# Performance work log

Measured on AMD Instinct MI355X. Metric: run time of the kernel, lower is better.

The kernel has to match this reference:

```python
import jax, jax.numpy as jnp
import numpy as np
import math

SIM_THRESHOLD = 0.05


def setup_inputs() -> dict:
    key = jax.random.key(0)
    ks = jax.random.split(key, 5)
    B, N, D = 32, 65, 512  # N = seq_len + 1
    gain = 1.0 / math.sqrt(2.0)
    lim = gain * math.sqrt(6.0 / (D + D))  # xavier_uniform with gain 1/sqrt(2)
    c = 1.0 / math.sqrt(D)
    return {
        "desc_embeddings": jax.random.normal(ks[0], (B, N - 1, D), jnp.float32),
        "name_value_embeddings": jax.random.normal(ks[1], (B, N, D), jnp.float32),
        "Wq": jax.random.uniform(ks[2], (D, D), jnp.float32, -lim, lim),
        "bq": jnp.zeros((D,), jnp.float32),
        "Wk": jax.random.uniform(ks[3], (D, D), jnp.float32, -lim, lim),
        "bk": jnp.zeros((D,), jnp.float32),
        "cls": jax.random.uniform(ks[4], (D,), jnp.float32, -c, c),
    }


def reference(desc_embeddings, name_value_embeddings, Wq, bq, Wk, bk, cls):
    # desc_embeddings is accepted but unused, exactly as in the torch module.
    nve = name_value_embeddings
    B, N, D = nve.shape
    S = N - 1

    q = nve @ Wq.T + bq  # [B, N, D]
    k = nve @ Wk.T + bk  # [B, N, D]
    attn = jnp.einsum('bid,bjd->bij', q, k) / math.sqrt(D)  # [B, N, N]

    # no_self_loop: multiplicatively zero the diagonal of the [1:,1:] block (pre-softmax)
    mask = jnp.ones((N, N), attn.dtype).at[1:, 1:].set(1.0 - jnp.eye(S, dtype=attn.dtype))
    attn = jax.nn.softmax(attn * mask, axis=-1)

    # row i's subgraph = {i} U {j : attn[b, i, j] > thr, j >= 1}
    members_all = (attn[:, 1:, 1:] > SIM_THRESHOLD) | jnp.eye(S, dtype=bool)  # [B, S, S]

    # Greedy sequential clustering: row i starts a subgraph only if node i is not
    # already used; its members then get marked used. Implemented with lax.scan
    # carrying the per-batch `used` bitmap (replaces the Python set loop).
    def step(used, xs):
        i, members = xs  # members: [B, S] for row i
        active = ~used[:, i]  # [B] -> is node (i+1) unused, i.e. this row is a leader
        sel = members & active[:, None]
        return used | sel, (active, sel)

    used0 = jnp.zeros((B, S), bool)
    _, (leader, member) = jax.lax.scan(
        step, used0, (jnp.arange(S), members_all.swapaxes(0, 1))
    )
    leader = leader.T.astype(nve.dtype)            # [B, S]
    member = member.transpose(1, 0, 2).astype(nve.dtype)  # [B, S, S]

    # Padded representation of the ragged output: for each leader row i,
    # slot 0 = cls token, slots 1..S = member embeddings (index order == sorted order),
    # zeros elsewhere. (out, leader_mask, member_mask) losslessly encode the
    # original list-of-lists of variable-size subgraphs.
    body = nve[:, None, 1:, :] * member[..., None]        # [B, S, S, D]
    cls_part = leader[:, :, None, None] * cls             # [B, S, 1, D]
    out = jnp.concatenate([cls_part, body], axis=2)       # [B, S, S+1, D]
    return out, leader, member
```

## Files before the change

### kernel.cpp

```cpp
#include <hip/hip_runtime.h>
#include <math.h>

constexpr int B = 32;
constexpr int N = 65;
constexpr int D = 512;
constexpr int S = 64;
constexpr int M = B * N;

constexpr size_t OUT0_ELEMS = (size_t)B * S * (S + 1) * D;
constexpr size_t Q_ELEMS    = (size_t)M * D;
constexpr size_t KT_ELEMS   = (size_t)B * D * N;
constexpr size_t STAGE_BASE = OUT0_ELEMS - Q_ELEMS - KT_ELEMS;
constexpr int OUT0_F4 = (int)(OUT0_ELEMS / 4);

constexpr int F_A = 6291456;
constexpr int F_B = 10485760;
constexpr int ROW_F4 = (S + 1) * (D / 4);
constexpr int ROWS_SCATTER = 1383;
constexpr int F_C = ROW_F4 * ROWS_SCATTER;

constexpr int NG_GEMM = 528;
constexpr int NG_FILL = 1536;
constexpr int N2_ATTN = 512;
constexpr int N2_FILL = 768;
constexpr int N3_FILL = 255;
constexpr int N4_DENSE = 2048;
constexpr int N4_TAIL  = 130;

__global__ __launch_bounds__(256) void k1_gemm_fill(
    const float* __restrict__ nve, const float* __restrict__ Wq,
    const float* __restrict__ bq, const float* __restrict__ Wk,
    const float* __restrict__ bk, float* __restrict__ out)
{
    __shared__ float As[32][68];
    __shared__ float Ws[32][68];

    const int gid = blockIdx.x;
    const int tid = threadIdx.x;

    if (gid < NG_GEMM) {
        const int mat = gid >= (NG_GEMM / 2);
        const int t   = mat ? gid - NG_GEMM / 2 : gid;
        const int bm  = (t % 33) * 64;
        const int bn  = (t / 33) * 64;
        const float* W    = mat ? Wk : Wq;
        const float* bias = mat ? bk : bq;

        float* q  = out + STAGE_BASE;
        float* kT = q + Q_ELEMS;

        const int tr = tid / 16;
        const int tc = tid % 16;
        float acc[4][4] = {};

        for (int k0 = 0; k0 < D; k0 += 32) {
            const int r  = tid / 8;
            const int c4 = (tid % 8) * 4;
            #pragma unroll
            for (int p = 0; p < 2; ++p) {
                const int rr = p * 32 + r;
                const int gm = bm + rr;
                float4 v = make_float4(0.f, 0.f, 0.f, 0.f);
                if (gm < M) v = *(const float4*)&nve[(size_t)gm * D + k0 + c4];
                As[c4 + 0][rr] = v.x; As[c4 + 1][rr] = v.y;
                As[c4 + 2][rr] = v.z; As[c4 + 3][rr] = v.w;
                float4 w = *(const float4*)&W[(size_t)(bn + rr) * D + k0 + c4];
                Ws[c4 + 0][rr] = w.x; Ws[c4 + 1][rr] = w.y;
                Ws[c4 + 2][rr] = w.z; Ws[c4 + 3][rr] = w.w;
            }
            __syncthreads();

            #pragma unroll
            for (int kk = 0; kk < 32; ++kk) {
                float a[4], w[4];
                #pragma unroll
                for (int u = 0; u < 4; ++u) a[u] = As[kk][tr * 4 + u];
                #pragma unroll
                for (int u = 0; u < 4; ++u) w[u] = Ws[kk][tc * 4 + u];
                #pragma unroll
                for (int i = 0; i < 4; ++i)
                    #pragma unroll
                    for (int j = 0; j < 4; ++j)
                        acc[i][j] += a[i] * w[j];
            }
            __syncthreads();
        }

        #pragma unroll
        for (int i = 0; i < 4; ++i) {
            const int gm = bm + tr * 4 + i;
            if (gm >= M) continue;
            const int b = gm / N;
            const int n = gm % N;
            if (mat == 0) {
                float4 v;
                v.x = acc[i][0] + bias[bn + tc * 4 + 0];
                v.y = acc[i][1] + bias[bn + tc * 4 + 1];
                v.z = acc[i][2] + bias[bn + tc * 4 + 2];
                v.w = acc[i][3] + bias[bn + tc * 4 + 3];
                *(float4*)&q[(size_t)gm * D + bn + tc * 4] = v;
            } else {
                #pragma unroll
                for (int j = 0; j < 4; ++j) {
                    const int gd = bn + tc * 4 + j;
                    kT[(size_t)b * D * N + (size_t)gd * N + n] = acc[i][j] + bias[gd];
                }
            }
        }
    } else {
        const float4 z = make_float4(0.f, 0.f, 0.f, 0.f);
        float4* o4 = (float4*)out;
        const int nthr = NG_FILL * 256;
        for (int f = (gid - NG_GEMM) * 256 + tid; f < F_A; f += nthr)
            o4[f] = z;
    }
}

__global__ __launch_bounds__(256) void k2_attn(
    const float* __restrict__ out, unsigned long long* __restrict__ mem,
    float* __restrict__ outw)
{
    const int gid = blockIdx.x;
    const int t = threadIdx.x;

    if (gid < N2_ATTN) {
        const float* q  = out + STAGE_BASE;
        const float* kT = q + Q_ELEMS;

        const int b = gid / 16;
        const int rbase = (gid % 16) * 4;

        __shared__ float qrow[4][D];
        __shared__ float sc[4][N];

        #pragma unroll
        for (int w = 0; w < 4; ++w) {
            if (t < 128) {
                const int i = rbase + w + 1;
                *(float4*)&qrow[w][t * 4] =
                    *(const float4*)&q[((size_t)b * N + i) * D + t * 4];
            }
        }
        __syncthreads();

        if (t < N) {
            const float* kp = &kT[(size_t)b * D * N];
            float a0 = 0.f, a1 = 0.f, a2 = 0.f, a3 = 0.f;
            for (int e = 0; e < D; ++e) {
                const float kv = kp[(size_t)e * N + t];
                a0 += qrow[0][e] * kv;
                a1 += qrow[1][e] * kv;
                a2 += qrow[2][e] * kv;
                a3 += qrow[3][e] * kv;
            }
            const float c = 0.044194173824159216f;
            float s0 = a0 * c, s1 = a1 * c, s2 = a2 * c, s3 = a3 * c;
            if (t == rbase + 1) s0 = 0.f;
            if (t == rbase + 2) s1 = 0.f;
            if (t == rbase + 3) s2 = 0.f;
            if (t == rbase + 4) s3 = 0.f;
            sc[0][t] = s0; sc[1][t] = s1; sc[2][t] = s2; sc[3][t] = s3;
        }
        __syncthreads();

        {
            const int w = t >> 6;
            const int lane = t & 63;
            const int i = rbase + w + 1;
            float mx = -INFINITY;
            for (int j = 0; j < N; ++j) mx = fmaxf(mx, sc[w][j]);
            float sum = 0.f;
            for (int j = 0; j < N; ++j) sum += expf(sc[w][j] - mx);
            const float p = expf(sc[w][lane + 1] - mx) / sum;
            const bool bit = (p > 0.05f) || (lane + 1 == i);
            unsigned long long mask = __ballot(bit);
            if (lane == 0) mem[b * S + rbase + w] = mask;
        }
    } else {
        const float4 z = make_float4(0.f, 0.f, 0.f, 0.f);
        float4* o4 = (float4*)outw;
        const int nthr = N2_FILL * 256;
        for (int f = F_A + (gid - N2_ATTN) * 256 + t; f < F_B; f += nthr)
            o4[f] = z;
    }
}

__global__ __launch_bounds__(256) void k3_cluster(
    const unsigned long long* __restrict__ mem,
    unsigned long long* __restrict__ sel,
    unsigned long long* __restrict__ lead,
    float* __restrict__ out)
{
    const int gid = blockIdx.x;
    const int t = threadIdx.x;
    if (gid == 0) {
        if (t >= B) return;
        const int b = t;
        unsigned long long used = 0ull, lb = 0ull;
        for (int i = 0; i < S; ++i) {
            const unsigned long long row = mem[b * S + i];
            const bool active = !((used >> i) & 1ull);
            const unsigned long long sl = active ? row : 0ull;
            used |= sl;
            lb |= (unsigned long long)active << i;
            sel[b * S + i] = sl;
        }
        lead[b] = lb;
    } else {
        const float4 z = make_float4(0.f, 0.f, 0.f, 0.f);
        float4* o4 = (float4*)out;
        const int nthr = N3_FILL * 256;
        for (int f = F_B + (gid - 1) * 256 + t; f < F_C; f += nthr)
            o4[f] = z;
    }
}

__global__ __launch_bounds__(256) void k4_finish(
    const float* __restrict__ nve, const float* __restrict__ cls,
    const unsigned long long* __restrict__ sel,
    const unsigned long long* __restrict__ lead,
    float* __restrict__ out)
{
    const int gid = blockIdx.x;
    const int t = threadIdx.x;

    if (gid < ROWS_SCATTER) {
        const int b = gid / S;
        const int i = gid % S;
        const unsigned long long lb = lead[b];
        const unsigned long long sb = sel[b * S + i];
        const int h = t >> 7;
        const int tt = t & 127;
        float4* slot0 = (float4*)(out + (((size_t)b * S + i) * (S + 1)) * D);
        for (int s = h; s <= S; s += 2) {
            bool on = (s == 0) ? ((lb >> i) & 1ull) : ((sb >> (s - 1)) & 1ull);
            if (!on) continue;
            const float* src = (s == 0) ? cls : &nve[((size_t)b * N + s) * D];
            slot0[(size_t)s * 128 + tt] = ((const float4*)src)[tt];
        }
    } else if (gid < ROWS_SCATTER + N4_DENSE) {
        float4* o4 = (float4*)out;
        const int nthr = N4_DENSE * 256;
        for (int f = F_C + (gid - ROWS_SCATTER) * 256 + t; f < OUT0_F4; f += nthr) {
            const int d4 = f & 127;
            const int slot = f >> 7;
            const int s = slot % (S + 1);
            const int row = slot / (S + 1);
            const int i = row % S;
            const int b = row / S;
            bool on;
            const float* src;
            if (s == 0) {
                on = (lead[b] >> i) & 1ull;
                src = &cls[d4 * 4];
            } else {
                on = (sel[b * S + i] >> (s - 1)) & 1ull;
                src = &nve[((size_t)b * N + s) * D + d4 * 4];
            }
            float4 v = make_float4(0.f, 0.f, 0.f, 0.f);
            if (on) v = *(const float4*)src;
            o4[f] = v;
        }
    } else {
        const int f = (gid - ROWS_SCATTER - N4_DENSE) * 256 + t;
        float* tail = out + OUT0_ELEMS;
        float4 v;
        #pragma unroll
        for (int c = 0; c < 4; ++c) {
            const int idx = f * 4 + c;
            float x;
            if (idx < B * S) {
                x = (float)((lead[idx / S] >> (idx % S)) & 1ull);
            } else {
                const int m = idx - B * S;
                const int b = m / (S * S);
                const int rem = m % (S * S);
                x = (float)((sel[b * S + rem / S] >> (rem % S)) & 1ull);
            }
            ((float*)&v)[c] = x;
        }
        *(float4*)&tail[(size_t)f * 4] = v;
    }
}

extern "C" void kernel_launch(void* const* d_in, const int* in_sizes, int n_in,
                              void* d_out, int out_size, void* d_ws, size_t ws_size,
                              hipStream_t stream) {
    const float* nve = (const float*)d_in[1];
    const float* Wq  = (const float*)d_in[2];
    const float* bq  = (const float*)d_in[3];
    const float* Wk  = (const float*)d_in[4];
    const float* bk  = (const float*)d_in[5];
    const float* cls = (const float*)d_in[6];

    float* out = (float*)d_out;

    unsigned long long* mem  = (unsigned long long*)d_ws;
    unsigned long long* sel  = mem + B * S;
    unsigned long long* lead = sel + B * S;

    k1_gemm_fill<<<NG_GEMM + NG_FILL, 256, 0, stream>>>(nve, Wq, bq, Wk, bk, out);
    k2_attn<<<N2_ATTN + N2_FILL, 256, 0, stream>>>(out, mem, out);
    k3_cluster<<<1 + N3_FILL, 256, 0, stream>>>(mem, sel, lead, out);
    k4_finish<<<ROWS_SCATTER + N4_DENSE + N4_TAIL, 256, 0, stream>>>(nve, cls, sel, lead, out);
}
```

Measured before the change: 116.5 us.

## Fuse Q/K projections, use wave-level softmax, and rebalance zero-fill work across kernels

The projection kernel now computes Q and K together in one block, sharing the loaded activation tile. It uses a 64-wide k-step, which halves the GEMM block count and the repeated activation reads. The attention kernel assigns two rows per wavefront and reduces the softmax with shuffles instead of serial shared-memory loops. The clustering kernel preloads the membership bitmasks into shared memory, and the zero-fill ranges and block counts are redistributed so more of the output is zeroed in earlier kernels and fewer dense blocks remain at the end. The risks are higher register and LDS pressure in the fused GEMM, and a load imbalance if the new fill split is off.

```diff
diff --git a/kernel.cpp b/kernel.cpp
--- a/kernel.cpp
+++ b/kernel.cpp
@@ -13,18 +13,18 @@
 constexpr size_t STAGE_BASE = OUT0_ELEMS - Q_ELEMS - KT_ELEMS;
 constexpr int OUT0_F4 = (int)(OUT0_ELEMS / 4);
 
-constexpr int F_A = 6291456;
-constexpr int F_B = 10485760;
 constexpr int ROW_F4 = (S + 1) * (D / 4);
-constexpr int ROWS_SCATTER = 1383;
+constexpr int ROWS_SCATTER = 1920;
 constexpr int F_C = ROW_F4 * ROWS_SCATTER;
-
-constexpr int NG_GEMM = 528;
+constexpr int F_A = 10000000;
+constexpr int F_B = 14400000;
+
+constexpr int NG_GEMM = 264;
 constexpr int NG_FILL = 1536;
-constexpr int N2_ATTN = 512;
+constexpr int N2_ATTN = 256;
 constexpr int N2_FILL = 768;
-constexpr int N3_FILL = 255;
-constexpr int N4_DENSE = 2048;
+constexpr int N3_FILL = 256;
+constexpr int N4_DENSE = 1024;
 constexpr int N4_TAIL  = 130;
 
 __global__ __launch_bounds__(256) void k1_gemm_fill(
@@ -32,56 +32,61 @@
     const float* __restrict__ bq, const float* __restrict__ Wk,
     const float* __restrict__ bk, float* __restrict__ out)
 {
-    __shared__ float As[32][68];
-    __shared__ float Ws[32][68];
+    __shared__ float As[64][68];
+    __shared__ float Qs[64][68];
+    __shared__ float Ks[64][68];
 
     const int gid = blockIdx.x;
     const int tid = threadIdx.x;
 
     if (gid < NG_GEMM) {
-        const int mat = gid >= (NG_GEMM / 2);
-        const int t   = mat ? gid - NG_GEMM / 2 : gid;
-        const int bm  = (t % 33) * 64;
-        const int bn  = (t / 33) * 64;
-        const float* W    = mat ? Wk : Wq;
-        const float* bias = mat ? bk : bq;
+        const int bm = (gid % 33) * 64;
+        const int bn = (gid / 33) * 64;
 
         float* q  = out + STAGE_BASE;
         float* kT = q + Q_ELEMS;
 
         const int tr = tid / 16;
         const int tc = tid % 16;
-        float acc[4][4] = {};
-
-        for (int k0 = 0; k0 < D; k0 += 32) {
-            const int r  = tid / 8;
-            const int c4 = (tid % 8) * 4;
+        float accq[4][4] = {};
+        float acck[4][4] = {};
+
+        for (int k0 = 0; k0 < D; k0 += 64) {
             #pragma unroll
-            for (int p = 0; p < 2; ++p) {
-                const int rr = p * 32 + r;
-                const int gm = bm + rr;
+            for (int p = 0; p < 4; ++p) {
+                const int idx = p * 256 + tid;
+                const int row = idx >> 4;
+                const int c4  = (idx & 15) * 4;
+                const int gm = bm + row;
                 float4 v = make_float4(0.f, 0.f, 0.f, 0.f);
                 if (gm < M) v = *(const float4*)&nve[(size_t)gm * D + k0 + c4];
-                As[c4 + 0][rr] = v.x; As[c4 + 1][rr] = v.y;
-                As[c4 + 2][rr] = v.z; As[c4 + 3][rr] = v.w;
-                float4 w = *(const float4*)&W[(size_t)(bn + rr) * D + k0 + c4];
-                Ws[c4 + 0][rr] = w.x; Ws[c4 + 1][rr] = w.y;
-                Ws[c4 + 2][rr] = w.z; Ws[c4 + 3][rr] = w.w;
+                As[c4 + 0][row] = v.x; As[c4 + 1][row] = v.y;
+                As[c4 + 2][row] = v.z; As[c4 + 3][row] = v.w;
+                float4 wq = *(const float4*)&Wq[(size_t)(bn + row) * D + k0 + c4];
+                Qs[c4 + 0][row] = wq.x; Qs[c4 + 1][row] = wq.y;
+                Qs[c4 + 2][row] = wq.z; Qs[c4 + 3][row] = wq.w;
+                float4 wk = *(const float4*)&Wk[(size_t)(bn + row) * D + k0 + c4];
+                Ks[c4 + 0][row] = wk.x; Ks[c4 + 1][row] = wk.y;
+                Ks[c4 + 2][row] = wk.z; Ks[c4 + 3][row] = wk.w;
             }
             __syncthreads();
 
-            #pragma unroll
-            for (int kk = 0; kk < 32; ++kk) {
-                float a[4], w[4];
+            #pragma unroll 8
+            for (int kk = 0; kk < 64; ++kk) {
+                float a[4], wq[4], wk[4];
                 #pragma unroll
-                for (int u = 0; u < 4; ++u) a[u] = As[kk][tr * 4 + u];
+                for (int u = 0; u < 4; ++u) a[u]  = As[kk][tr * 4 + u];
                 #pragma unroll
-                for (int u = 0; u < 4; ++u) w[u] = Ws[kk][tc * 4 + u];
+                for (int u = 0; u < 4; ++u) wq[u] = Qs[kk][tc * 4 + u];
+                #pragma unroll
+                for (int u = 0; u < 4; ++u) wk[u] = Ks[kk][tc * 4 + u];
                 #pragma unroll
                 for (int i = 0; i < 4; ++i)
                     #pragma unroll
-                    for (int j = 0; j < 4; ++j)
-                        acc[i][j] += a[i] * w[j];
+                    for (int j = 0; j < 4; ++j) {
+                        accq[i][j] += a[i] * wq[j];
+                        acck[i][j] += a[i] * wk[j];
+                    }
             }
             __syncthreads();
         }
@@ -92,19 +97,16 @@
             if (gm >= M) continue;
             const int b = gm / N;
             const int n = gm % N;
-            if (mat == 0) {
-                float4 v;
-                v.x = acc[i][0] + bias[bn + tc * 4 + 0];
-                v.y = acc[i][1] + bias[bn + tc * 4 + 1];
-                v.z = acc[i][2] + bias[bn + tc * 4 + 2];
-                v.w = acc[i][3] + bias[bn + tc * 4 + 3];
-                *(float4*)&q[(size_t)gm * D + bn + tc * 4] = v;
-            } else {
-                #pragma unroll
-                for (int j = 0; j < 4; ++j) {
-                    const int gd = bn + tc * 4 + j;
-                    kT[(size_t)b * D * N + (size_t)gd * N + n] = acc[i][j] + bias[gd];
-                }
+            float4 v;
+            v.x = accq[i][0] + bq[bn + tc * 4 + 0];
+            v.y = accq[i][1] + bq[bn + tc * 4 + 1];
+            v.z = accq[i][2] + bq[bn + tc * 4 + 2];
+            v.w = accq[i][3] + bq[bn + tc * 4 + 3];
+            *(float4*)&q[(size_t)gm * D + bn + tc * 4] = v;
+            #pragma unroll
+            for (int j = 0; j < 4; ++j) {
+                const int gd = bn + tc * 4 + j;
+                kT[(size_t)b * D * N + (size_t)gd * N + n] = acck[i][j] + bk[gd];
             }
         }
     } else {
@@ -127,54 +129,58 @@
         const float* q  = out + STAGE_BASE;
         const float* kT = q + Q_ELEMS;
 
-        const int b = gid / 16;
-        const int rbase = (gid % 16) * 4;
-
-        __shared__ float qrow[4][D];
-        __shared__ float sc[4][N];
-
-        #pragma unroll
-        for (int w = 0; w < 4; ++w) {
-            if (t < 128) {
-                const int i = rbase + w + 1;
-                *(float4*)&qrow[w][t * 4] =
-                    *(const float4*)&q[((size_t)b * N + i) * D + t * 4];
-            }
+        const int b  = gid >> 3;
+        const int r0 = (gid & 7) * 8;
+
+        __shared__ float qs[8][D];
+
+        #pragma unroll
+        for (int p = 0; p < 4; ++p) {
+            const int idx = p * 256 + t;
+            const int rl  = idx >> 7;
+            const int d4  = idx & 127;
+            const int i   = r0 + rl + 1;
+            *(float4*)&qs[rl][d4 * 4] =
+                *(const float4*)&q[((size_t)b * N + i) * D + d4 * 4];
         }
         __syncthreads();
 
-        if (t < N) {
-            const float* kp = &kT[(size_t)b * D * N];
-            float a0 = 0.f, a1 = 0.f, a2 = 0.f, a3 = 0.f;
-            for (int e = 0; e < D; ++e) {
-                const float kv = kp[(size_t)e * N + t];
-                a0 += qrow[0][e] * kv;
-                a1 += qrow[1][e] * kv;
-                a2 += qrow[2][e] * kv;
-                a3 += qrow[3][e] * kv;
-            }
-            const float c = 0.044194173824159216f;
-            float s0 = a0 * c, s1 = a1 * c, s2 = a2 * c, s3 = a3 * c;
-            if (t == rbase + 1) s0 = 0.f;
-            if (t == rbase + 2) s1 = 0.f;
-            if (t == rbase + 3) s2 = 0.f;
-            if (t == rbase + 4) s3 = 0.f;
-            sc[0][t] = s0; sc[1][t] = s1; sc[2][t] = s2; sc[3][t] = s3;
-        }
-        __syncthreads();
-
-        {
-            const int w = t >> 6;
-            const int lane = t & 63;
-            const int i = rbase + w + 1;
-            float mx = -INFINITY;
-            for (int j = 0; j < N; ++j) mx = fmaxf(mx, sc[w][j]);
-            float sum = 0.f;
-            for (int j = 0; j < N; ++j) sum += expf(sc[w][j] - mx);
-            const float p = expf(sc[w][lane + 1] - mx) / sum;
-            const bool bit = (p > 0.05f) || (lane + 1 == i);
+        const int w = t >> 6;
+        const int l = t & 63;
+        const int rA = w * 2, rB = w * 2 + 1;
+        const int iA = r0 + rA + 1, iB = r0 + rB + 1;
+
+        const float* kp = &kT[(size_t)b * D * N];
+        float aA = 0.f, aB = 0.f, a0A = 0.f, a0B = 0.f;
+        #pragma unroll 4
+        for (int d = 0; d < D; ++d) {
+            const float kv0 = kp[d * N];
+            const float kv  = kp[d * N + 1 + l];
+            const float qa  = qs[rA][d];
+            const float qb  = qs[rB][d];
+            aA  += qa * kv;  aB  += qb * kv;
+            a0A += qa * kv0; a0B += qb * kv0;
+        }
+
+        const float c = 0.044194173824159216f;
+        #pragma unroll
+        for (int pass = 0; pass < 2; ++pass) {
+            const int i = pass ? iB : iA;
+            float s  = (pass ? aB : aA) * c;
+            const float s0 = (pass ? a0B : a0A) * c;
+            if (l == i - 1) s = 0.f;
+            float m = s;
+            #pragma unroll
+            for (int off = 32; off; off >>= 1) m = fmaxf(m, __shfl_xor(m, off));
+            m = fmaxf(m, s0);
+            float e = expf(s - m);
+            float sum = e;
+            #pragma unroll
+            for (int off = 32; off; off >>= 1) sum += __shfl_xor(sum, off);
+            sum += expf(s0 - m);
+            const bool bit = (e / sum > 0.05f) || (l == i - 1);
             unsigned long long mask = __ballot(bit);
-            if (lane == 0) mem[b * S + rbase + w] = mask;
+            if (l == 0) mem[b * S + i - 1] = mask;
         }
     } else {
         const float4 z = make_float4(0.f, 0.f, 0.f, 0.f);
@@ -194,18 +200,23 @@
     const int gid = blockIdx.x;
     const int t = threadIdx.x;
     if (gid == 0) {
-        if (t >= B) return;
-        const int b = t;
-        unsigned long long used = 0ull, lb = 0ull;
-        for (int i = 0; i < S; ++i) {
-            const unsigned long long row = mem[b * S + i];
-            const bool active = !((used >> i) & 1ull);
-            const unsigned long long sl = active ? row : 0ull;
-            used |= sl;
-            lb |= (unsigned long long)active << i;
-            sel[b * S + i] = sl;
-        }
-        lead[b] = lb;
+        __shared__ unsigned long long lmem[B * S];
+        #pragma unroll
+        for (int p = 0; p < 8; ++p) lmem[p * 256 + t] = mem[p * 256 + t];
+        __syncthreads();
+        if (t < B) {
+            const int b = t;
+            unsigned long long used = 0ull, lb = 0ull;
+            for (int i = 0; i < S; ++i) {
+                const unsigned long long row = lmem[b * S + i];
+                const bool active = !((used >> i) & 1ull);
+                const unsigned long long sl = active ? row : 0ull;
+                used |= sl;
+                lb |= (unsigned long long)active << i;
+                sel[b * S + i] = sl;
+            }
+            lead[b] = lb;
+        }
     } else {
         const float4 z = make_float4(0.f, 0.f, 0.f, 0.f);
         float4* o4 = (float4*)out;
@@ -225,8 +236,8 @@
     const int t = threadIdx.x;
 
     if (gid < ROWS_SCATTER) {
-        const int b = gid / S;
-        const int i = gid % S;
+        const int b = gid >> 6;
+        const int i = gid & 63;
         const unsigned long long lb = lead[b];
         const unsigned long long sb = sel[b * S + i];
         const int h = t >> 7;
@@ -246,8 +257,8 @@
             const int slot = f >> 7;
             const int s = slot % (S + 1);
             const int row = slot / (S + 1);
-            const int i = row % S;
-            const int b = row / S;
+            const int i = row & 63;
+            const int b = row >> 6;
             bool on;
             const float* src;
             if (s == 0) {
```

Measured after the change: 151.8 us. 30.3% more time.
